# Optimization experiments

Hardware: AMD Instinct MI355X
Metric: run time of the kernel (lower is better)

## Reference

```python
import jax, jax.numpy as jnp
import numpy as np

IMG_SIZE = 640
NUM_CLASSES = 80
KA = 3
STRIDES = (8, 16, 32)
CONF_THRESH = 0.001
NMS_THRESH = 0.6
ANCHORS = np.array([[12, 16], [19, 36], [40, 28],
                    [36, 75], [76, 55], [72, 146],
                    [142, 110], [192, 243], [459, 401]], np.float32).reshape(3, 3, 2)
CLS_OFFSET = 4.0  # > max normalized coord (1.0); separates classes for class-wise NMS


def _make_grid(stride):
    f = IMG_SIZE // stride
    gy, gx = jnp.meshgrid(jnp.arange(f), jnp.arange(f), indexing='ij')
    # [HW, 1, 2] in (x, y) order, row-major over (H, W) like permute(1,2,0).view(-1,...)
    return jnp.stack([gx, gy], axis=-1).reshape(-1, 1, 2).astype(jnp.float32)


def _decode_level(pred, level):
    # pred: [KA*(1+C+4), H, W] -> obj [HW*KA,1], cls [HW*KA,C], boxes [HW*KA,4]
    C = NUM_CLASSES
    p = jnp.transpose(pred, (1, 2, 0)).reshape(-1, KA * (1 + C + 4))  # [HW, ch]
    obj = p[:, :KA].reshape(-1, 1)
    cls = p[:, KA:KA * (1 + C)].reshape(-1, C)
    reg = p[:, KA * (1 + C):].reshape(-1, KA, 4)
    grid = _make_grid(STRIDES[level])               # [HW, 1, 2]
    anchors = jnp.asarray(ANCHORS[level])           # [KA, 2]
    xy = (jax.nn.sigmoid(reg[..., :2]) + grid) * STRIDES[level]
    wh = jnp.exp(reg[..., 2:]) * anchors
    box = jnp.concatenate([xy - wh * 0.5, xy + wh * 0.5], axis=-1).reshape(-1, 4)
    return obj, cls, box


def _greedy_nms(boxes, scores, valid, thresh):
    # Faithful sequential greedy NMS (same math as the numpy loop), via lax.scan.
    N = boxes.shape[0]
    order = jnp.argsort(-scores)
    b = boxes[order]
    v = valid[order]
    areas = (b[:, 2] - b[:, 0]) * (b[:, 3] - b[:, 1])
    idx = jnp.arange(N)

    def step(suppressed, i):
        keep_i = v[i] & jnp.logical_not(suppressed[i])
        xx1 = jnp.maximum(b[i, 0], b[:, 0])
        yy1 = jnp.maximum(b[i, 1], b[:, 1])
        xx2 = jnp.minimum(b[i, 2], b[:, 2])
        yy2 = jnp.minimum(b[i, 3], b[:, 3])
        w = jnp.maximum(1e-28, xx2 - xx1)
        h = jnp.maximum(1e-28, yy2 - yy1)
        inter = w * h
        ovr = inter / (areas[i] + areas - inter + 1e-14)
        suppressed = suppressed | (keep_i & (ovr > thresh) & (idx > i))
        return suppressed, keep_i

    _, kept_sorted = jax.lax.scan(step, jnp.zeros(N, bool), idx)
    return jnp.zeros(N, bool).at[order].set(kept_sorted)


def _forward(pred_s, pred_m, pred_l):
    outs = [_decode_level(p, i) for i, p in enumerate((pred_s, pred_m, pred_l))]
    obj = jnp.concatenate([o[0] for o in outs], axis=0)   # [N, 1]
    cls = jnp.concatenate([o[1] for o in outs], axis=0)   # [N, C]
    box = jnp.concatenate([o[2] for o in outs], axis=0)   # [N, 4]
    bboxes = jnp.clip(box / IMG_SIZE, 0.0, 1.0)
    scores = jax.nn.sigmoid(obj) * jax.nn.softmax(cls, axis=-1)  # [N, C]
    cls_inds = jnp.argmax(scores, axis=1)
    conf = jnp.max(scores, axis=1)
    valid = conf >= CONF_THRESH
    # per-class NMS == class-offset trick: different classes never overlap
    nms_boxes = bboxes + cls_inds.astype(bboxes.dtype)[:, None] * CLS_OFFSET
    keep = _greedy_nms(jax.lax.stop_gradient(nms_boxes),
                       jax.lax.stop_gradient(conf), valid, NMS_THRESH)
    return bboxes, conf, cls_inds, keep


def setup_inputs() -> dict:
    key = jax.random.key(0)
    k1, k2, k3 = jax.random.split(key, 3)
    ch = KA * (1 + NUM_CLASSES + 4)  # 255
    return {
        'pred_s': jax.random.normal(k1, (ch, 80, 80), jnp.float32),
        'pred_m': jax.random.normal(k2, (ch, 40, 40), jnp.float32),
        'pred_l': jax.random.normal(k3, (ch, 20, 20), jnp.float32),
    }


def reference(pred_s, pred_m, pred_l):
    # returns fixed-shape (bboxes [N,4], scores [N], cls_inds [N], keep mask [N])
    return _forward(pred_s, pred_m, pred_l)
```

## Files before the change

### kernel.cpp

```cpp
#include <hip/hip_runtime.h>

typedef unsigned long long u64;
typedef unsigned int u32;

#define N_TOT 25200
#define NCLS 80
#define CAP 512

__device__ __constant__ float c_AW[9] = {12.f,19.f,40.f,36.f,76.f,72.f,142.f,192.f,459.f};
__device__ __constant__ float c_AH[9] = {16.f,36.f,28.f,75.f,55.f,146.f,110.f,243.f,401.f};

__global__ __launch_bounds__(256)
void decode_kernel(const float* __restrict__ p0,
                   const float* __restrict__ p1,
                   const float* __restrict__ p2,
                   float* __restrict__ out)
{
    const int t = blockIdx.x * 256 + threadIdx.x;
    const int n = t >> 2;
    const int q = t & 3;
    if (n >= N_TOT) return;

    const float* p; int f, strd, base, lvl;
    if (n < 19200)      { p = p0; f = 80; strd = 8;  base = 0;     lvl = 0; }
    else if (n < 24000) { p = p1; f = 40; strd = 16; base = 19200; lvl = 1; }
    else                { p = p2; f = 20; strd = 32; base = 24000; lvl = 2; }

    const int r  = n - base;
    const int hw = r / 3;
    const int a  = r - hw * 3;
    const int HW = f * f;
    const int gx = hw % f;
    const int gy = hw / f;
    const float* cell = p + hw;
    const float* clsp = cell + (3 + a * NCLS) * HW;
    const float* regp = cell + (243 + a * 4) * HW;

    const float rv  = regp[q * HW];
    const float obj = cell[a * HW];

    float v[20];
    #pragma unroll
    for (int k = 0; k < 20; ++k) v[k] = clsp[(4 * k + q) * HW];

    float lmax = v[0];
    #pragma unroll
    for (int k = 1; k < 20; ++k) lmax = fmaxf(lmax, v[k]);
    float gm = lmax;
    gm = fmaxf(gm, __shfl_xor(gm, 1));
    gm = fmaxf(gm, __shfl_xor(gm, 2));

    float ls = 0.f, bp = -1.f; int ba_ = 0;
    #pragma unroll
    for (int k = 0; k < 20; ++k) {
        float pc = expf(v[k] - gm);
        ls += pc;
        if (pc > bp) { bp = pc; ba_ = 4 * k + q; }
    }
    float gs = ls;
    gs += __shfl_xor(gs, 1);
    gs += __shfl_xor(gs, 2);
    {
        float bp2; int ba2;
        bp2 = __shfl_xor(bp, 1); ba2 = __shfl_xor(ba_, 1);
        if (bp2 > bp || (bp2 == bp && ba2 < ba_)) { bp = bp2; ba_ = ba2; }
        bp2 = __shfl_xor(bp, 2); ba2 = __shfl_xor(ba_, 2);
        if (bp2 > bp || (bp2 == bp && ba2 < ba_)) { bp = bp2; ba_ = ba2; }
    }

    const int lane = threadIdx.x & 63;
    const int gb = lane & 60;
    const float tx = __shfl(rv, gb);
    const float ty = __shfl(rv, gb + 1);
    const float tw = __shfl(rv, gb + 2);
    const float th = __shfl(rv, gb + 3);

    if (q != 0) return;

    float sig  = 1.f / (1.f + expf(-obj));
    float conf = sig * (bp / gs);

    float sx = 1.f / (1.f + expf(-tx));
    float sy = 1.f / (1.f + expf(-ty));
    float cx = (sx + (float)gx) * (float)strd;
    float cy = (sy + (float)gy) * (float)strd;
    const int ai = lvl * 3 + a;
    float w  = expf(tw) * c_AW[ai];
    float h  = expf(th) * c_AH[ai];
    float hx = w * 0.5f, hy = h * 0.5f;
    float x1 = (cx - hx) / 640.0f;
    float y1 = (cy - hy) / 640.0f;
    float x2 = (cx + hx) / 640.0f;
    float y2 = (cy + hy) / 640.0f;
    x1 = fminf(fmaxf(x1, 0.f), 1.f);
    y1 = fminf(fmaxf(y1, 0.f), 1.f);
    x2 = fminf(fmaxf(x2, 0.f), 1.f);
    y2 = fminf(fmaxf(y2, 0.f), 1.f);

    *(float4*)(out + n * 4) = make_float4(x1, y1, x2, y2);
    out[100800 + n] = conf;
    out[126000 + n] = (float)ba_;
    out[151200 + n] = 0.0f;
}

__global__ __launch_bounds__(1024)
void nms_kernel(const float* __restrict__ out,
                float* __restrict__ out_keep)
{
    const int c = blockIdx.x;
    const int tid = threadIdx.x;
    const int wave = tid >> 6, lane = tid & 63;

    __shared__ int    scnt;
    __shared__ u64    skey[CAP];
    __shared__ float4 sbox[CAP + 1];
    __shared__ int    sgi[CAP];
    __shared__ u64    maskT[8 * CAP];

    if (tid == 0) scnt = 0;
    __syncthreads();

    const float* confp = out + 100800;
    const float* clsp  = out + 126000;
    float4 cf[7], cl[7];
    bool   inb[7];
    #pragma unroll
    for (int itr = 0; itr < 7; ++itr) {
        const int ib = itr * 1024 + tid;
        inb[itr] = (ib < 6300);
        if (inb[itr]) {
            cf[itr] = *(const float4*)(confp + ib * 4);
            cl[itr] = *(const float4*)(clsp  + ib * 4);
        } else {
            cf[itr] = make_float4(-1.f, -1.f, -1.f, -1.f);
            cl[itr] = make_float4(0.f, 0.f, 0.f, 0.f);
        }
    }
    const u64 lt = (1ull << lane) - 1ull;
    #pragma unroll
    for (int itr = 0; itr < 7; ++itr) {
        const bool m0 = inb[itr] && ((int)cl[itr].x == c) && (cf[itr].x >= 0.001f);
        const bool m1 = inb[itr] && ((int)cl[itr].y == c) && (cf[itr].y >= 0.001f);
        const bool m2 = inb[itr] && ((int)cl[itr].z == c) && (cf[itr].z >= 0.001f);
        const bool m3 = inb[itr] && ((int)cl[itr].w == c) && (cf[itr].w >= 0.001f);
        const u64 b0 = __ballot(m0), b1 = __ballot(m1), b2 = __ballot(m2), b3 = __ballot(m3);
        const int t0 = __popcll(b0), t1 = __popcll(b1), t2 = __popcll(b2), t3 = __popcll(b3);
        const int tot = t0 + t1 + t2 + t3;
        if (tot) {
            int bs = 0;
            if (lane == 0) bs = atomicAdd(&scnt, tot);
            bs = __shfl(bs, 0);
            const int i0 = itr * 4096 + tid * 4;
            int pos;
            if (m0) { pos = bs + __popcll(b0 & lt);
                      if (pos < CAP) skey[pos] = ((u64)__float_as_uint(cf[itr].x) << 32) | (u64)(~(u32)(i0)); }
            if (m1) { pos = bs + t0 + __popcll(b1 & lt);
                      if (pos < CAP) skey[pos] = ((u64)__float_as_uint(cf[itr].y) << 32) | (u64)(~(u32)(i0 + 1)); }
            if (m2) { pos = bs + t0 + t1 + __popcll(b2 & lt);
                      if (pos < CAP) skey[pos] = ((u64)__float_as_uint(cf[itr].z) << 32) | (u64)(~(u32)(i0 + 2)); }
            if (m3) { pos = bs + t0 + t1 + t2 + __popcll(b3 & lt);
                      if (pos < CAP) skey[pos] = ((u64)__float_as_uint(cf[itr].w) << 32) | (u64)(~(u32)(i0 + 3)); }
        }
    }
    __syncthreads();
    const int M  = min(scnt, CAP);
    const int MW = (M + 63) >> 6;

    if (wave < MW) {
        const int e = (wave << 6) + lane;
        if (e < M) {
            const u64 ke = skey[e];
            int rank = 0;
            int j = 0;
            for (; j + 16 <= M; j += 16) {
                rank += (int)(skey[j]    > ke) + (int)(skey[j+1]  > ke)
                      + (int)(skey[j+2]  > ke) + (int)(skey[j+3]  > ke)
                      + (int)(skey[j+4]  > ke) + (int)(skey[j+5]  > ke)
                      + (int)(skey[j+6]  > ke) + (int)(skey[j+7]  > ke)
                      + (int)(skey[j+8]  > ke) + (int)(skey[j+9]  > ke)
                      + (int)(skey[j+10] > ke) + (int)(skey[j+11] > ke)
                      + (int)(skey[j+12] > ke) + (int)(skey[j+13] > ke)
                      + (int)(skey[j+14] > ke) + (int)(skey[j+15] > ke);
            }
            for (; j < M; ++j) rank += (int)(skey[j] > ke);

            const u32 gi = ~(u32)ke;
            const float4 b = *(const float4*)(out + gi * 4);
            const float off = 4.0f * (float)c;
            sbox[rank] = make_float4(b.x + off, b.y + off, b.z + off, b.w + off);
            sgi[rank]  = (int)gi;
        }
    }
    __syncthreads();

#define IOU_BIT(RB, I) {                                                \
        const float ra = ((RB).z - (RB).x) * ((RB).w - (RB).y);         \
        float xx1 = fmaxf((RB).x, cb.x);                                \
        float yy1 = fmaxf((RB).y, cb.y);                                \
        float xx2 = fminf((RB).z, cb.z);                                \
        float yy2 = fminf((RB).w, cb.w);                                \
        float ww = fmaxf(1e-28f, xx2 - xx1);                            \
        float hh = fmaxf(1e-28f, yy2 - yy1);                            \
        float inter = ww * hh;                                          \
        float ovr = inter / (ra + ca - inter + 1e-14f);                 \
        bits |= (u64)(((I) < j) && (ovr >= 0.6f)) << ((I) & 63);        \
    }
    const int ntiles = (MW * (MW + 1)) >> 1;
    for (int tt = wave; tt < ntiles; tt += 16) {
        int rw = 0, acc = 0;
        while (tt >= acc + (MW - rw)) { acc += MW - rw; ++rw; }
        const int cw = rw + (tt - acc);
        const int j  = (cw << 6) + lane;
        const float4 cb = sbox[min(j, M - 1)];
        const float  ca = (cb.z - cb.x) * (cb.w - cb.y);
        const int r0 = rw << 6;
        const int r1 = min(r0 + 64, M);
        u64 bits = 0ull;
        int i = r0;
        for (; i + 4 <= r1; i += 4) {
            const float4 b0 = sbox[i];
            const float4 b1 = sbox[i + 1];
            const float4 b2 = sbox[i + 2];
            const float4 b3 = sbox[i + 3];
            IOU_BIT(b0, i) IOU_BIT(b1, i + 1) IOU_BIT(b2, i + 2) IOU_BIT(b3, i + 3)
        }
        for (; i < r1; ++i) {
            const float4 b0 = sbox[i];
            IOU_BIT(b0, i)
        }
        maskT[rw * CAP + j] = bits;
    }
#undef IOU_BIT
    __syncthreads();

    if (wave != 0) return;

    u64 k0 = 0, k1 = 0, k2 = 0, k3 = 0, k4 = 0, k5 = 0, k6 = 0, k7 = 0;
    (void)k7;
#define MT(W) maskT[(W) * CAP + j]
#define TILE(W, PRE)                                                    \
    if ((W) < MW) {                                                     \
        const int j = ((W) << 6) + lane;                                \
        const u64 mine = MT(W);                                         \
        const u64 pre = (PRE);                                          \
        const int rm = M - ((W) << 6);                                  \
        const u64 valid = (rm >= 64) ? ~0ull : ((1ull << rm) - 1ull);   \
        u64 cand = valid & ~__ballot(pre != 0ull);                      \
        u64 kept = 0ull;                                                \
        while (cand) {                                                  \
            const u64 remv = cand & __ballot((mine & kept) != 0ull);    \
            cand &= ~remv;                                              \
            const u64 newk = cand & __ballot((mine & cand) == 0ull);    \
            kept |= newk;                                               \
            cand &= ~newk;                                              \
        }                                                               \
        k##W = kept;                                                    \
        if ((kept >> lane) & 1ull) out_keep[sgi[j]] = 1.0f;             \
    }
    TILE(0, 0ull)
    TILE(1, (MT(0)&k0))
    TILE(2, (MT(0)&k0)|(MT(1)&k1))
    TILE(3, (MT(0)&k0)|(MT(1)&k1)|(MT(2)&k2))
    TILE(4, (MT(0)&k0)|(MT(1)&k1)|(MT(2)&k2)|(MT(3)&k3))
    TILE(5, (MT(0)&k0)|(MT(1)&k1)|(MT(2)&k2)|(MT(3)&k3)|(MT(4)&k4))
    TILE(6, (MT(0)&k0)|(MT(1)&k1)|(MT(2)&k2)|(MT(3)&k3)|(MT(4)&k4)|(MT(5)&k5))
    TILE(7, (MT(0)&k0)|(MT(1)&k1)|(MT(2)&k2)|(MT(3)&k3)|(MT(4)&k4)|(MT(5)&k5)|(MT(6)&k6))
#undef TILE
#undef MT
}

extern "C" void kernel_launch(void* const* d_in, const int* in_sizes, int n_in,
                              void* d_out, int out_size, void* d_ws, size_t ws_size,
                              hipStream_t stream) {
    const float* p0 = (const float*)d_in[0];
    const float* p1 = (const float*)d_in[1];
    const float* p2 = (const float*)d_in[2];
    float* out = (float*)d_out;

    decode_kernel<<<(N_TOT * 4 + 255) / 256, 256, 0, stream>>>(p0, p1, p2, out);
    nms_kernel<<<NCLS, 1024, 0, stream>>>(out, out + 151200);
}
```

Measured before the change: 43.85 us.

## Decode one anchor per thread with anchor-major mapping for coalesced loads

The decode kernel now assigns one thread per (anchor, cell) and orders threads anchor-major within each level, so neighbouring threads read neighbouring spatial positions and every channel load is coalesced. Each thread loads all 80 class logits and reduces them alone, which removes the four-lane shuffle reductions. Blocks shrink to 64 threads. The price is higher register pressure from the 80-element array, fewer threads for latency hiding, and scattered output writes, since the output index n is still cell-major.

```diff
diff --git a/kernel.cpp b/kernel.cpp
--- a/kernel.cpp
+++ b/kernel.cpp
@@ -10,84 +10,61 @@
 __device__ __constant__ float c_AW[9] = {12.f,19.f,40.f,36.f,76.f,72.f,142.f,192.f,459.f};
 __device__ __constant__ float c_AH[9] = {16.f,36.f,28.f,75.f,55.f,146.f,110.f,243.f,401.f};
 
-__global__ __launch_bounds__(256)
+__global__ __launch_bounds__(64)
 void decode_kernel(const float* __restrict__ p0,
                    const float* __restrict__ p1,
                    const float* __restrict__ p2,
                    float* __restrict__ out)
 {
-    const int t = blockIdx.x * 256 + threadIdx.x;
-    const int n = t >> 2;
-    const int q = t & 3;
-    if (n >= N_TOT) return;
-
-    const float* p; int f, strd, base, lvl;
-    if (n < 19200)      { p = p0; f = 80; strd = 8;  base = 0;     lvl = 0; }
-    else if (n < 24000) { p = p1; f = 40; strd = 16; base = 19200; lvl = 1; }
-    else                { p = p2; f = 20; strd = 32; base = 24000; lvl = 2; }
-
-    const int r  = n - base;
-    const int hw = r / 3;
-    const int a  = r - hw * 3;
+    const int m = blockIdx.x * 64 + threadIdx.x;
+    if (m >= N_TOT) return;
+
+    const float* p; int f, strd, base, ml;
+    int lvl;
+    if (m < 19200)      { p = p0; f = 80; strd = 8;  base = 0;     lvl = 0; ml = m; }
+    else if (m < 24000) { p = p1; f = 40; strd = 16; base = 19200; lvl = 1; ml = m - 19200; }
+    else                { p = p2; f = 20; strd = 32; base = 24000; lvl = 2; ml = m - 24000; }
     const int HW = f * f;
+    const int a  = ml / HW;
+    const int hw = ml - a * HW;
     const int gx = hw % f;
     const int gy = hw / f;
     const float* cell = p + hw;
+
     const float* clsp = cell + (3 + a * NCLS) * HW;
+    float v[80];
+    #pragma unroll
+    for (int c = 0; c < 80; ++c) v[c] = clsp[c * HW];
+    const float obj = cell[a * HW];
     const float* regp = cell + (243 + a * 4) * HW;
-
-    const float rv  = regp[q * HW];
-    const float obj = cell[a * HW];
-
-    float v[20];
-    #pragma unroll
-    for (int k = 0; k < 20; ++k) v[k] = clsp[(4 * k + q) * HW];
-
-    float lmax = v[0];
-    #pragma unroll
-    for (int k = 1; k < 20; ++k) lmax = fmaxf(lmax, v[k]);
-    float gm = lmax;
-    gm = fmaxf(gm, __shfl_xor(gm, 1));
-    gm = fmaxf(gm, __shfl_xor(gm, 2));
-
-    float ls = 0.f, bp = -1.f; int ba_ = 0;
-    #pragma unroll
-    for (int k = 0; k < 20; ++k) {
-        float pc = expf(v[k] - gm);
-        ls += pc;
-        if (pc > bp) { bp = pc; ba_ = 4 * k + q; }
-    }
-    float gs = ls;
-    gs += __shfl_xor(gs, 1);
-    gs += __shfl_xor(gs, 2);
-    {
-        float bp2; int ba2;
-        bp2 = __shfl_xor(bp, 1); ba2 = __shfl_xor(ba_, 1);
-        if (bp2 > bp || (bp2 == bp && ba2 < ba_)) { bp = bp2; ba_ = ba2; }
-        bp2 = __shfl_xor(bp, 2); ba2 = __shfl_xor(ba_, 2);
-        if (bp2 > bp || (bp2 == bp && ba2 < ba_)) { bp = bp2; ba_ = ba2; }
-    }
-
-    const int lane = threadIdx.x & 63;
-    const int gb = lane & 60;
-    const float tx = __shfl(rv, gb);
-    const float ty = __shfl(rv, gb + 1);
-    const float tw = __shfl(rv, gb + 2);
-    const float th = __shfl(rv, gb + 3);
-
-    if (q != 0) return;
-
-    float sig  = 1.f / (1.f + expf(-obj));
-    float conf = sig * (bp / gs);
-
-    float sx = 1.f / (1.f + expf(-tx));
-    float sy = 1.f / (1.f + expf(-ty));
-    float cx = (sx + (float)gx) * (float)strd;
-    float cy = (sy + (float)gy) * (float)strd;
+    const float tx = regp[0];
+    const float ty = regp[HW];
+    const float tw = regp[2 * HW];
+    const float th = regp[3 * HW];
+
+    float gm = v[0];
+    #pragma unroll
+    for (int c = 1; c < 80; ++c) gm = fmaxf(gm, v[c]);
+    float gs = 0.f, bp = -1.f; int ba_ = 0;
+    #pragma unroll
+    for (int c = 0; c < 80; ++c) {
+        const float pc = expf(v[c] - gm);
+        gs += pc;
+        if (pc > bp) { bp = pc; ba_ = c; }
+    }
+
+    const float sig  = 1.f / (1.f + expf(-obj));
+    const float conf = sig * (bp / gs);
+    const int n = base + hw * 3 + a;
+
+    const float sx = 1.f / (1.f + expf(-tx));
+    const float sy = 1.f / (1.f + expf(-ty));
+    const float cx = (sx + (float)gx) * (float)strd;
+    const float cy = (sy + (float)gy) * (float)strd;
     const int ai = lvl * 3 + a;
-    float w  = expf(tw) * c_AW[ai];
-    float h  = expf(th) * c_AH[ai];
-    float hx = w * 0.5f, hy = h * 0.5f;
+    const float w  = expf(tw) * c_AW[ai];
+    const float h  = expf(th) * c_AH[ai];
+    const float hx = w * 0.5f, hy = h * 0.5f;
     float x1 = (cx - hx) / 640.0f;
     float y1 = (cy - hy) / 640.0f;
     float x2 = (cx + hx) / 640.0f;
@@ -277,6 +254,6 @@
     const float* p2 = (const float*)d_in[2];
     float* out = (float*)d_out;
 
-    decode_kernel<<<(N_TOT * 4 + 255) / 256, 256, 0, stream>>>(p0, p1, p2, out);
+    decode_kernel<<<(N_TOT + 63) / 64, 64, 0, stream>>>(p0, p1, p2, out);
     nms_kernel<<<NCLS, 1024, 0, stream>>>(out, out + 151200);
 }
```

New measurement: 44.16 us. About the same (+0.7%).

## Rank NMS keys via register readlane broadcast and force early batched loads

Applied to the files above, without the earlier changes.

Replaces the per-lane LDS scan over all sorted keys with a wave-level scheme: each wave loads 64-key chunks into registers and broadcasts them via readlane so every lane compares against uniform values. It also adds empty asm barriers so the global and LDS loads in the decode, gather and IoU loops are issued as a batch before any use, overlapping their latency. The readlane path costs 64 scalar reads per chunk, and the asm barriers raise register pressure.

```diff
diff --git a/kernel.cpp b/kernel.cpp
--- a/kernel.cpp
+++ b/kernel.cpp
@@ -9,6 +9,12 @@
 
 __device__ __constant__ float c_AW[9] = {12.f,19.f,40.f,36.f,76.f,72.f,142.f,192.f,459.f};
 __device__ __constant__ float c_AH[9] = {16.f,36.f,28.f,75.f,55.f,146.f,110.f,243.f,401.f};
+
+__device__ __forceinline__ u64 rdlane64(u64 v, int l) {
+    u32 lo = __builtin_amdgcn_readlane((u32)v, l);
+    u32 hi = __builtin_amdgcn_readlane((u32)(v >> 32), l);
+    return ((u64)hi << 32) | (u64)lo;
+}
 
 __global__ __launch_bounds__(256)
 void decode_kernel(const float* __restrict__ p0,
@@ -36,12 +42,15 @@
     const float* clsp = cell + (3 + a * NCLS) * HW;
     const float* regp = cell + (243 + a * 4) * HW;
 
-    const float rv  = regp[q * HW];
-    const float obj = cell[a * HW];
+    float rv  = regp[q * HW];
+    float obj = cell[a * HW];
 
     float v[20];
     #pragma unroll
     for (int k = 0; k < 20; ++k) v[k] = clsp[(4 * k + q) * HW];
+    #pragma unroll
+    for (int k = 0; k < 20; ++k) asm volatile("" : "+v"(v[k]));
+    asm volatile("" : "+v"(rv), "+v"(obj));
 
     float lmax = v[0];
     #pragma unroll
@@ -128,13 +137,17 @@
     for (int itr = 0; itr < 7; ++itr) {
         const int ib = itr * 1024 + tid;
         inb[itr] = (ib < 6300);
+        cf[itr] = make_float4(-1.f, -1.f, -1.f, -1.f);
+        cl[itr] = make_float4(0.f, 0.f, 0.f, 0.f);
         if (inb[itr]) {
             cf[itr] = *(const float4*)(confp + ib * 4);
             cl[itr] = *(const float4*)(clsp  + ib * 4);
-        } else {
-            cf[itr] = make_float4(-1.f, -1.f, -1.f, -1.f);
-            cl[itr] = make_float4(0.f, 0.f, 0.f, 0.f);
-        }
+        }
+    }
+    #pragma unroll
+    for (int itr = 0; itr < 7; ++itr) {
+        asm volatile("" : "+v"(cf[itr].x), "+v"(cf[itr].y), "+v"(cf[itr].z), "+v"(cf[itr].w),
+                          "+v"(cl[itr].x), "+v"(cl[itr].y), "+v"(cl[itr].z), "+v"(cl[itr].w));
     }
     const u64 lt = (1ull << lane) - 1ull;
     #pragma unroll
@@ -168,22 +181,22 @@
 
     if (wave < MW) {
         const int e = (wave << 6) + lane;
+        u64 kw0 = 0, kw1 = 0, kw2 = 0, kw3 = 0, kw4 = 0, kw5 = 0, kw6 = 0, kw7 = 0;
+#define LOADK(W2) if ((W2) < MW) { const int ix = ((W2) << 6) + lane; kw##W2 = (ix < M) ? skey[ix] : 0ull; }
+        LOADK(0) LOADK(1) LOADK(2) LOADK(3) LOADK(4) LOADK(5) LOADK(6) LOADK(7)
+#undef LOADK
+        asm volatile("" : "+v"(kw0), "+v"(kw1), "+v"(kw2), "+v"(kw3),
+                          "+v"(kw4), "+v"(kw5), "+v"(kw6), "+v"(kw7));
+        const u64 ke = (e < M) ? skey[e] : ~0ull;
+        int rank = 0;
+#define RANKW(W2) if ((W2) < MW) {                                      \
+            _Pragma("unroll 8")                                         \
+            for (int l = 0; l < 64; ++l)                                \
+                rank += (int)(rdlane64(kw##W2, l) > ke);                \
+        }
+        RANKW(0) RANKW(1) RANKW(2) RANKW(3) RANKW(4) RANKW(5) RANKW(6) RANKW(7)
+#undef RANKW
         if (e < M) {
-            const u64 ke = skey[e];
-            int rank = 0;
-            int j = 0;
-            for (; j + 16 <= M; j += 16) {
-                rank += (int)(skey[j]    > ke) + (int)(skey[j+1]  > ke)
-                      + (int)(skey[j+2]  > ke) + (int)(skey[j+3]  > ke)
-                      + (int)(skey[j+4]  > ke) + (int)(skey[j+5]  > ke)
-                      + (int)(skey[j+6]  > ke) + (int)(skey[j+7]  > ke)
-                      + (int)(skey[j+8]  > ke) + (int)(skey[j+9]  > ke)
-                      + (int)(skey[j+10] > ke) + (int)(skey[j+11] > ke)
-                      + (int)(skey[j+12] > ke) + (int)(skey[j+13] > ke)
-                      + (int)(skey[j+14] > ke) + (int)(skey[j+15] > ke);
-            }
-            for (; j < M; ++j) rank += (int)(skey[j] > ke);
-
             const u32 gi = ~(u32)ke;
             const float4 b = *(const float4*)(out + gi * 4);
             const float off = 4.0f * (float)c;
@@ -218,10 +231,14 @@
         u64 bits = 0ull;
         int i = r0;
         for (; i + 4 <= r1; i += 4) {
-            const float4 b0 = sbox[i];
-            const float4 b1 = sbox[i + 1];
-            const float4 b2 = sbox[i + 2];
-            const float4 b3 = sbox[i + 3];
+            float4 b0 = sbox[i];
+            float4 b1 = sbox[i + 1];
+            float4 b2 = sbox[i + 2];
+            float4 b3 = sbox[i + 3];
+            asm volatile("" : "+v"(b0.x), "+v"(b0.y), "+v"(b0.z), "+v"(b0.w),
+                              "+v"(b1.x), "+v"(b1.y), "+v"(b1.z), "+v"(b1.w),
+                              "+v"(b2.x), "+v"(b2.y), "+v"(b2.z), "+v"(b2.w),
+                              "+v"(b3.x), "+v"(b3.y), "+v"(b3.z), "+v"(b3.w));
             IOU_BIT(b0, i) IOU_BIT(b1, i + 1) IOU_BIT(b2, i + 2) IOU_BIT(b3, i + 3)
         }
         for (; i < r1; ++i) {
```

New measurement: 51.40 us. 1.17x slower.
